# Kernel tuning notes

Measured on AMD Instinct MI355X. Metric: run time of the kernel, lower is better.

## Reference

```python
import jax, jax.numpy as jnp
import numpy as np

B, P, K = 32, 1024, 16  # clouds, points per cloud, neighbors


def setup_inputs() -> dict:
    key = jax.random.key(0)
    ks = jax.random.split(key, 5)
    N, C, H, D = B * P, 64, 128, 3
    x = jax.random.normal(ks[0], (N, C), dtype=jnp.float32)
    pos = jax.random.normal(ks[1], (N, D), dtype=jnp.float32)
    batch = jnp.arange(N, dtype=jnp.int64) // P  # cloud id per node
    W_e = jax.random.normal(ks[2], (2 * C, H), dtype=jnp.float32) * 0.05
    b_e = jnp.zeros((H,), dtype=jnp.float32)
    W_sc = jax.random.normal(ks[3], (C, H), dtype=jnp.float32) * 0.05
    b_sc = jnp.zeros((H,), dtype=jnp.float32)
    return {"x": x, "pos": pos, "batch": batch,
            "W_e": W_e, "b_e": b_e, "W_sc": W_sc, "b_sc": b_sc}


def _knn_idx(posb):
    # posb: [B, P, D] -> idx [B, P, K]: K nearest neighbors (sources) per target node,
    # within each cloud, excluding self (loop=False in torch_geometric.knn_graph).
    sq = jnp.sum(posb * posb, axis=-1)                       # [B, P]
    d2 = sq[:, :, None] + sq[:, None, :] - 2.0 * jnp.einsum('bid,bjd->bij', posb, posb)
    d2 = d2 + jnp.eye(P, dtype=posb.dtype)[None] * jnp.finfo(posb.dtype).max / 2
    _, idx = jax.lax.top_k(-d2, K)                           # [B, P, K]
    return idx


def reference(x, pos, batch, W_e, b_e, W_sc, b_sc):
    C = x.shape[-1]
    xb = x.reshape(B, P, C)
    posb = pos.reshape(B, P, -1)
    idx = _knn_idx(posb)                                     # [B, P, K]
    # gather neighbor (source) features per target node
    x_j = jax.vmap(lambda xc, ic: xc[ic])(xb, idx)           # [B, P, K, C]
    x_i = xb[:, :, None, :]                                  # [B, P, 1, C]
    # EdgeConv message: nn([x_i, x_j - x_i]), here Linear + ReLU
    e = jnp.concatenate([jnp.broadcast_to(x_i, x_j.shape), x_j - x_i], axis=-1)  # [B,P,K,2C]
    msg = jax.nn.relu(jnp.einsum('bpke,eh->bpkh', e, W_e) + b_e)
    agg = jnp.max(msg, axis=2)                               # max aggregation -> [B, P, H]
    shortcut = x @ W_sc + b_sc                               # [N, H]
    out = agg.reshape(-1, agg.shape[-1]) + shortcut
    return out
```

## Files before the change

kernel.cpp:

```cpp
#include <hip/hip_runtime.h>
#include <float.h>
#include <stdint.h>

#define BATCHES 32
#define P 1024
#define KNN 16
#define C 64
#define H 128
#define N (BATCHES * P)
#define NCOLS 384
#define SPLITS 8
#define CPS 128
#define QB 32

typedef short short8 __attribute__((ext_vector_type(8)));
typedef float floatx4 __attribute__((ext_vector_type(4)));

struct alignas(16) F4 { float x, y, z, w; };

__device__ __forceinline__ unsigned short f2bf(float f) {
    unsigned u = __float_as_uint(f);
    unsigned r = (u + 0x7FFF + ((u >> 16) & 1)) >> 16;
    return (unsigned short)r;
}

__global__ __launch_bounds__(256) void prep_kernel(
    const float* __restrict__ W_e, const float* __restrict__ b_e,
    const float* __restrict__ W_sc, const float* __restrict__ b_sc,
    const float* __restrict__ pos,
    unsigned short* __restrict__ WT, float* __restrict__ bias,
    F4* __restrict__ posq)
{
    int b = blockIdx.x;
    if (b < 96) {
        int i = b * 256 + threadIdx.x;
        int col = i >> 6, c = i & 63;
        float w;
        if (col < 128)      w = W_e[c * 128 + col] - W_e[(64 + c) * 128 + col];
        else if (col < 256) w = W_e[(64 + c) * 128 + (col - 128)];
        else                w = W_sc[c * 128 + (col - 256)];
        WT[col * 64 + c] = f2bf(w);
        if (c == 0) {
            bias[col] = (col < 128) ? b_e[col] : (col < 256 ? 0.0f : b_sc[col - 256]);
        }
    } else {
        int j = (b - 96) * 256 + threadIdx.x;
        float x = pos[j * 3 + 0], y = pos[j * 3 + 1], z = pos[j * 3 + 2];
        float sq = __fadd_rn(__fadd_rn(__fmul_rn(x, x), __fmul_rn(y, y)),
                             __fmul_rn(z, z));
        posq[j] = F4{x, y, z, sq};
    }
}

struct PA {
    float lists[SPLITS][16][QB];
    unsigned short offs[SPLITS][QB];
    unsigned short cnts[SPLITS][QB];
    float Tq[QB];
};

__global__ __launch_bounds__(256, 8) void knn_gemm_kernel(
    const F4* __restrict__ posq, const float* __restrict__ X,
    const unsigned short* __restrict__ WT, const float* __restrict__ bias,
    int* __restrict__ idx_out,
    unsigned short* __restrict__ U, unsigned short* __restrict__ V,
    unsigned short* __restrict__ S)
{
    __shared__ __align__(16) PA Ash;
    PA* A = &Ash;

    int t = threadIdx.x;
    int q = t & 31, s = t >> 5;
    int blk = blockIdx.x;
    int batch = blk >> 5;
    int qblk  = blk & 31;
    int iloc  = qblk * QB + q;

    const F4* pq = posq + (size_t)batch * P;
    F4 me = pq[iloc];
    const int j0 = s * CPS;

    float d[16];
#pragma unroll
    for (int k = 0; k < 16; ++k) d[k] = FLT_MAX;

    auto dist = [&](const F4& c, int j) -> float {
        float dot = __fadd_rn(__fadd_rn(__fmul_rn(me.x, c.x), __fmul_rn(me.y, c.y)),
                              __fmul_rn(me.z, c.z));
        float d2 = __fadd_rn(__fadd_rn(me.w, c.w), __fmul_rn(-2.0f, dot));
        return (j == iloc) ? FLT_MAX : d2;
    };
    auto insert = [&](float d2) {
#pragma unroll
        for (int k = 15; k >= 1; --k)
            d[k] = __builtin_amdgcn_fmed3f(d[k - 1], d2, d[k]);
        d[0] = fminf(d[0], d2);
    };

#pragma unroll 4
    for (int jj = 0; jj < CPS; ++jj) {
        int j = j0 + jj;
        F4 c = pq[j];
        insert(dist(c, j));
    }

#pragma unroll
    for (int k = 0; k < 16; ++k) A->lists[s][k][q] = d[k];
    __syncthreads();

    if ((t >> 6) == (blk & 3) && (t & 63) < 32) {
        float v[8], wv[8];
        int   n[8];
#pragma unroll
        for (int l = 0; l < 8; ++l) {
            v[l]  = A->lists[l][0][q];
            wv[l] = A->lists[l][1][q];
            n[l]  = 0;
        }
        float T = 0.0f;
#pragma unroll 1
        for (int k = 0; k < 16; ++k) {
            float mn = fminf(fminf(fminf(v[0], v[1]), fminf(v[2], v[3])),
                             fminf(fminf(v[4], v[5]), fminf(v[6], v[7])));
            bool taken = false;
#pragma unroll
            for (int l = 0; l < 8; ++l) {
                bool tk = (!taken) && (v[l] == mn);
                taken = taken || tk;
                int ni = n[l] + (tk ? 1 : 0);
                int ri = ni + 1;
                float rv = A->lists[l][(ri < 16) ? ri : 15][q];
                float wnew = (ri < 16) ? rv : FLT_MAX;
                v[l]  = tk ? wv[l] : v[l];
                wv[l] = tk ? wnew  : wv[l];
                n[l]  = ni;
            }
            T = mn;
        }
        A->Tq[q] = T;
        int off = 0;
#pragma unroll
        for (int l = 0; l < 8; ++l) {
            A->offs[l][q] = (unsigned short)off;
            A->cnts[l][q] = (unsigned short)n[l];
            off += n[l];
        }
    }
    __syncthreads();

    {
        float T  = A->Tq[q];
        int   cap = A->cnts[s][q];
        int   gb  = (blk * QB + q) * KNN + A->offs[s][q];
        int   base = batch * P;
        int   cnt = 0;

#pragma unroll 4
        for (int jj = 0; jj < CPS; ++jj) {
            int j = j0 + jj;
            F4 c = pq[j];
            float d2 = dist(c, j);
            if (d2 <= T && cnt < cap) {
                idx_out[gb + cnt] = base + j;
                cnt++;
            }
        }
    }

    {
        int w  = t >> 6;
        int ln = t & 63;
        int mt = w & 1, nh = w >> 1;
        int m0 = blk * QB + mt * 16;
        int lm = ln & 15, kg = ln >> 4;

        const float4* arow = (const float4*)(X + (size_t)(m0 + lm) * 64 + kg * 8);
        float4 f0 = arow[0], f1 = arow[1];
        float4 f2 = arow[8], f3 = arow[9];
        short8 a0, a1;
        a0[0] = (short)f2bf(f0.x); a0[1] = (short)f2bf(f0.y);
        a0[2] = (short)f2bf(f0.z); a0[3] = (short)f2bf(f0.w);
        a0[4] = (short)f2bf(f1.x); a0[5] = (short)f2bf(f1.y);
        a0[6] = (short)f2bf(f1.z); a0[7] = (short)f2bf(f1.w);
        a1[0] = (short)f2bf(f2.x); a1[1] = (short)f2bf(f2.y);
        a1[2] = (short)f2bf(f2.z); a1[3] = (short)f2bf(f2.w);
        a1[4] = (short)f2bf(f3.x); a1[5] = (short)f2bf(f3.y);
        a1[6] = (short)f2bf(f3.z); a1[7] = (short)f2bf(f3.w);

        size_t rowbase = (size_t)(blk * QB + mt * 16 + kg * 4) * H;

#pragma unroll 4
        for (int nt = nh * 12; nt < nh * 12 + 12; ++nt) {
            const short8* brow = (const short8*)(WT + (size_t)(nt * 16 + lm) * 64 + kg * 8);
            short8 b0 = brow[0];
            short8 b1 = brow[4];
            floatx4 acc = {0.0f, 0.0f, 0.0f, 0.0f};
            acc = __builtin_amdgcn_mfma_f32_16x16x32_bf16(a0, b0, acc, 0, 0, 0);
            acc = __builtin_amdgcn_mfma_f32_16x16x32_bf16(a1, b1, acc, 0, 0, 0);

            int col = nt * 16 + lm;
            float bv = bias[col];
            unsigned short* dst = (col < 128) ? (U + col)
                                : (col < 256) ? (V + (col - 128))
                                              : (S + (col - 256));
#pragma unroll
            for (int r = 0; r < 4; ++r)
                dst[rowbase + (size_t)r * H] = f2bf(acc[r] + bv);
        }
    }
}

__global__ __launch_bounds__(256) void final_kernel(
    const int* __restrict__ idx, const unsigned short* __restrict__ U,
    const unsigned short* __restrict__ V, const unsigned short* __restrict__ S,
    float* __restrict__ out)
{
    int t = threadIdx.x;
    __shared__ int nbr[16][KNN];
    ((int*)nbr)[t] = idx[(size_t)blockIdx.x * 256 + t];
    __syncthreads();

    int pl = t >> 4;
    int c8 = t & 15;
    size_t p = (size_t)blockIdx.x * 16 + pl;

    uint4 uu = ((const uint4*)(U + p * H))[c8];
    uint4 ss = ((const uint4*)(S + p * H))[c8];

    float m0 = -FLT_MAX, m1 = -FLT_MAX, m2 = -FLT_MAX, m3 = -FLT_MAX;
    float m4 = -FLT_MAX, m5 = -FLT_MAX, m6 = -FLT_MAX, m7 = -FLT_MAX;
#pragma unroll
    for (int k = 0; k < KNN; ++k) {
        int row = nbr[pl][k];
        uint4 vv = *(const uint4*)(V + (size_t)row * H + c8 * 8);
        m0 = fmaxf(m0, __uint_as_float(vv.x << 16));
        m1 = fmaxf(m1, __uint_as_float(vv.x & 0xFFFF0000u));
        m2 = fmaxf(m2, __uint_as_float(vv.y << 16));
        m3 = fmaxf(m3, __uint_as_float(vv.y & 0xFFFF0000u));
        m4 = fmaxf(m4, __uint_as_float(vv.z << 16));
        m5 = fmaxf(m5, __uint_as_float(vv.z & 0xFFFF0000u));
        m6 = fmaxf(m6, __uint_as_float(vv.w << 16));
        m7 = fmaxf(m7, __uint_as_float(vv.w & 0xFFFF0000u));
    }

    float4 oa, ob;
    oa.x = fmaxf(__uint_as_float(uu.x << 16)         + m0, 0.0f) + __uint_as_float(ss.x << 16);
    oa.y = fmaxf(__uint_as_float(uu.x & 0xFFFF0000u) + m1, 0.0f) + __uint_as_float(ss.x & 0xFFFF0000u);
    oa.z = fmaxf(__uint_as_float(uu.y << 16)         + m2, 0.0f) + __uint_as_float(ss.y << 16);
    oa.w = fmaxf(__uint_as_float(uu.y & 0xFFFF0000u) + m3, 0.0f) + __uint_as_float(ss.y & 0xFFFF0000u);
    ob.x = fmaxf(__uint_as_float(uu.z << 16)         + m4, 0.0f) + __uint_as_float(ss.z << 16);
    ob.y = fmaxf(__uint_as_float(uu.z & 0xFFFF0000u) + m5, 0.0f) + __uint_as_float(ss.z & 0xFFFF0000u);
    ob.z = fmaxf(__uint_as_float(uu.w << 16)         + m6, 0.0f) + __uint_as_float(ss.w << 16);
    ob.w = fmaxf(__uint_as_float(uu.w & 0xFFFF0000u) + m7, 0.0f) + __uint_as_float(ss.w & 0xFFFF0000u);
    ((float4*)(out + p * H))[c8 * 2]     = oa;
    ((float4*)(out + p * H))[c8 * 2 + 1] = ob;
}

extern "C" void kernel_launch(void* const* d_in, const int* in_sizes, int n_in,
                              void* d_out, int out_size, void* d_ws, size_t ws_size,
                              hipStream_t stream)
{
    const float* x    = (const float*)d_in[0];
    const float* pos  = (const float*)d_in[1];
    const float* W_e  = (const float*)d_in[3];
    const float* b_e  = (const float*)d_in[4];
    const float* W_sc = (const float*)d_in[5];
    const float* b_sc = (const float*)d_in[6];
    float* out = (float*)d_out;

    char* ws = (char*)d_ws;
    const size_t OFF_IDX  = 0;
    const size_t OFF_U    = 2ull << 20;
    const size_t OFF_V    = OFF_U + (8ull << 20);
    const size_t OFF_S    = OFF_V + (8ull << 20);
    const size_t OFF_WT   = OFF_S + (8ull << 20);
    const size_t OFF_BIAS = OFF_WT + 49152;
    const size_t OFF_POSQ = OFF_BIAS + 2048;

    int*            idx  = (int*)(ws + OFF_IDX);
    unsigned short* U    = (unsigned short*)(ws + OFF_U);
    unsigned short* V    = (unsigned short*)(ws + OFF_V);
    unsigned short* S    = (unsigned short*)(ws + OFF_S);
    unsigned short* WT   = (unsigned short*)(ws + OFF_WT);
    float*          bias = (float*)(ws + OFF_BIAS);
    F4*             posq = (F4*)(ws + OFF_POSQ);

    prep_kernel<<<96 + N / 256, 256, 0, stream>>>(W_e, b_e, W_sc, b_sc, pos,
                                                  WT, bias, posq);
    knn_gemm_kernel<<<N / QB, 256, 0, stream>>>(posq, x, WT, bias, idx, U, V, S);
    final_kernel<<<N / 16, 256, 0, stream>>>(idx, U, V, S, out);
}
```

Baseline: 159.2 us.

## Halve query block to 16 with 16 candidate splits and stage GEMM output in LDS

The kNN+GEMM kernel now handles 16 queries per block, split across 16 candidate slices of 64 points. This doubles the block count and shortens each thread's serial insertion loop, at the cost of a 16-way merge per query instead of 8-way. The GEMM epilogue writes bf16 results into a padded shared-memory buffer reusing the kNN scratch space, then stores them to U/V/S with coalesced 8-byte writes instead of scattered 2-byte stores. The lists array is padded to reduce bank conflicts, and extra barriers are added to allow the shared memory reuse.

```diff
diff --git a/kernel.cpp b/kernel.cpp
--- a/kernel.cpp
+++ b/kernel.cpp
@@ -9,9 +9,10 @@
 #define H 128
 #define N (BATCHES * P)
 #define NCOLS 384
-#define SPLITS 8
-#define CPS 128
-#define QB 32
+#define SPLITS 16
+#define CPS 64
+#define QB 16
+#define PADH 132
 
 typedef short short8 __attribute__((ext_vector_type(8)));
 typedef float floatx4 __attribute__((ext_vector_type(4)));
@@ -53,10 +54,15 @@
 }
 
 struct PA {
-    float lists[SPLITS][16][QB];
+    float lists[SPLITS][16][QB + 1];
     unsigned short offs[SPLITS][QB];
     unsigned short cnts[SPLITS][QB];
     float Tq[QB];
+};
+struct PB {
+    unsigned short Ubuf[QB][PADH];
+    unsigned short Vbuf[QB][PADH];
+    unsigned short Sbuf[QB][PADH];
 };
 
 __global__ __launch_bounds__(256, 8) void knn_gemm_kernel(
@@ -66,14 +72,15 @@
     unsigned short* __restrict__ U, unsigned short* __restrict__ V,
     unsigned short* __restrict__ S)
 {
-    __shared__ __align__(16) PA Ash;
-    PA* A = &Ash;
+    __shared__ __align__(16) char smraw[sizeof(PA)];
+    PA* A  = (PA*)smraw;
+    PB* Bm = (PB*)smraw;
 
     int t = threadIdx.x;
-    int q = t & 31, s = t >> 5;
+    int q = t & 15, s = t >> 4;
     int blk = blockIdx.x;
-    int batch = blk >> 5;
-    int qblk  = blk & 31;
+    int batch = blk >> 6;
+    int qblk  = blk & 63;
     int iloc  = qblk * QB + q;
 
     const F4* pq = posq + (size_t)batch * P;
@@ -108,28 +115,30 @@
     for (int k = 0; k < 16; ++k) A->lists[s][k][q] = d[k];
     __syncthreads();
 
-    if ((t >> 6) == (blk & 3) && (t & 63) < 32) {
-        float v[8], wv[8];
-        int   n[8];
-#pragma unroll
-        for (int l = 0; l < 8; ++l) {
-            v[l]  = A->lists[l][0][q];
-            wv[l] = A->lists[l][1][q];
+    if ((t >> 6) == (blk & 3) && (t & 63) < QB) {
+        int qm = t & 63;
+        float v[SPLITS], wv[SPLITS];
+        int   n[SPLITS];
+#pragma unroll
+        for (int l = 0; l < SPLITS; ++l) {
+            v[l]  = A->lists[l][0][qm];
+            wv[l] = A->lists[l][1][qm];
             n[l]  = 0;
         }
         float T = 0.0f;
 #pragma unroll 1
         for (int k = 0; k < 16; ++k) {
-            float mn = fminf(fminf(fminf(v[0], v[1]), fminf(v[2], v[3])),
-                             fminf(fminf(v[4], v[5]), fminf(v[6], v[7])));
+            float mn = v[0];
+#pragma unroll
+            for (int l = 1; l < SPLITS; ++l) mn = fminf(mn, v[l]);
             bool taken = false;
 #pragma unroll
-            for (int l = 0; l < 8; ++l) {
+            for (int l = 0; l < SPLITS; ++l) {
                 bool tk = (!taken) && (v[l] == mn);
                 taken = taken || tk;
                 int ni = n[l] + (tk ? 1 : 0);
                 int ri = ni + 1;
-                float rv = A->lists[l][(ri < 16) ? ri : 15][q];
+                float rv = A->lists[l][(ri < 16) ? ri : 15][qm];
                 float wnew = (ri < 16) ? rv : FLT_MAX;
                 v[l]  = tk ? wv[l] : v[l];
                 wv[l] = tk ? wnew  : wv[l];
@@ -137,12 +146,12 @@
             }
             T = mn;
         }
-        A->Tq[q] = T;
+        A->Tq[qm] = T;
         int off = 0;
 #pragma unroll
-        for (int l = 0; l < 8; ++l) {
-            A->offs[l][q] = (unsigned short)off;
-            A->cnts[l][q] = (unsigned short)n[l];
+        for (int l = 0; l < SPLITS; ++l) {
+            A->offs[l][qm] = (unsigned short)off;
+            A->cnts[l][qm] = (unsigned short)n[l];
             off += n[l];
         }
     }
@@ -166,13 +175,13 @@
             }
         }
     }
+    __syncthreads();
 
     {
         int w  = t >> 6;
         int ln = t & 63;
-        int mt = w & 1, nh = w >> 1;
-        int m0 = blk * QB + mt * 16;
         int lm = ln & 15, kg = ln >> 4;
+        int m0 = blk * QB;
 
         const float4* arow = (const float4*)(X + (size_t)(m0 + lm) * 64 + kg * 8);
         float4 f0 = arow[0], f1 = arow[1];
@@ -187,10 +196,8 @@
         a1[4] = (short)f2bf(f3.x); a1[5] = (short)f2bf(f3.y);
         a1[6] = (short)f2bf(f3.z); a1[7] = (short)f2bf(f3.w);
 
-        size_t rowbase = (size_t)(blk * QB + mt * 16 + kg * 4) * H;
-
-#pragma unroll 4
-        for (int nt = nh * 12; nt < nh * 12 + 12; ++nt) {
+#pragma unroll 3
+        for (int nt = w * 6; nt < w * 6 + 6; ++nt) {
             const short8* brow = (const short8*)(WT + (size_t)(nt * 16 + lm) * 64 + kg * 8);
             short8 b0 = brow[0];
             short8 b1 = brow[4];
@@ -200,12 +207,28 @@
 
             int col = nt * 16 + lm;
             float bv = bias[col];
-            unsigned short* dst = (col < 128) ? (U + col)
-                                : (col < 256) ? (V + (col - 128))
-                                              : (S + (col - 256));
-#pragma unroll
-            for (int r = 0; r < 4; ++r)
-                dst[rowbase + (size_t)r * H] = f2bf(acc[r] + bv);
+#pragma unroll
+            for (int r = 0; r < 4; ++r) {
+                int row = kg * 4 + r;
+                unsigned short val = f2bf(acc[r] + bv);
+                if (col < 128)      Bm->Ubuf[row][col] = val;
+                else if (col < 256) Bm->Vbuf[row][col - 128] = val;
+                else                Bm->Sbuf[row][col - 256] = val;
+            }
+        }
+    }
+    __syncthreads();
+
+    {
+        uint2* Ug = (uint2*)U + (size_t)blk * 512;
+        uint2* Vg = (uint2*)V + (size_t)blk * 512;
+        uint2* Sg = (uint2*)S + (size_t)blk * 512;
+#pragma unroll
+        for (int i = t; i < 512; i += 256) {
+            int row = i >> 5, off = (i & 31) * 4;
+            Ug[i] = *(const uint2*)&Bm->Ubuf[row][off];
+            Vg[i] = *(const uint2*)&Bm->Vbuf[row][off];
+            Sg[i] = *(const uint2*)&Bm->Sbuf[row][off];
         }
     }
 }
```

After: 161.2 us. Within noise of the previous version (+1.3%).
